# Performance work log

Hardware: AMD Instinct MI355X
Metric: run time of the kernel (lower is better)

The kernel has to match this reference:

```python
import jax, jax.numpy as jnp
import numpy as np

EPS = 1e-7  # K.epsilon()


def setup_inputs() -> dict:
    key = jax.random.key(0)
    k1, k2, k3 = jax.random.split(key, 3)
    B, T, D = 64, 2048, 256
    x = jax.random.normal(k1, (B, T, D), dtype=jnp.float32)
    W = jax.random.normal(k2, (D, D), dtype=jnp.float32) * (1.0 / np.sqrt(D))
    b = jnp.zeros((D,), dtype=jnp.float32)
    uw = jax.random.normal(k3, (D,), dtype=jnp.float32) * (1.0 / np.sqrt(D))
    mask = jnp.ones((B, T), dtype=jnp.int32)
    return {"x": x, "W": W, "b": b, "uw": uw, "mask": mask}


def reference(x, W, b, uw, mask):
    # x: [B, T, D]; W: [D, D]; b, uw: [D]; mask: [B, T]
    eij = jnp.tanh(jnp.einsum('btd,de->bte', x, W) + b)   # [B, T, D]
    eij = jnp.einsum('btd,d->bt', eij, uw)                # [B, T]
    a = jnp.exp(eij) * mask.astype(x.dtype)               # [B, T]
    a = a / (jnp.sum(a, axis=1, keepdims=True) + EPS)     # normalize over time
    return jnp.einsum('btd,bt->bd', x, a)                 # [B, D]
```

## Files before the change

### kernel.cpp

```cpp
#include <hip/hip_runtime.h>
#include <hip/hip_bf16.h>

#define BB 64
#define TT 2048
#define DD 256
#define EPSF 1e-7f
#define ROWS 32
#define XS_STRIDE 264

typedef __attribute__((ext_vector_type(8))) short v8s;
typedef __attribute__((ext_vector_type(4))) float v4f;

__device__ __forceinline__ float bf2f(unsigned short u) {
    union { unsigned int i; float f; } c;
    c.i = ((unsigned int)u) << 16;
    return c.f;
}

__device__ __forceinline__ unsigned int pack2_bf16(float a, float b) {
    union { __hip_bfloat162 h; unsigned int u; } c;
    c.h = __float22bfloat162_rn(make_float2(a, b));
    return c.u;
}

__device__ __forceinline__ float tanh_fast(float x) {
    float e = __expf(2.0f * x);
    return 1.0f - 2.0f / (e + 1.0f);
}

__device__ __forceinline__ unsigned short f2bf_rn(float f) {
    union { __hip_bfloat16 h; unsigned short u; } c;
    c.h = __float2bfloat16(f);
    return c.u;
}

__global__ __launch_bounds__(256) void pack_wt_frag(const float* __restrict__ W,
                                                    unsigned short* __restrict__ Wt) {
    int idx = blockIdx.x * 256 + threadIdx.x;
    int j    = idx & 7;
    int quad = (idx >> 3) & 3;
    int m    = (idx >> 5) & 15;
    int ks   = (idx >> 9) & 7;
    int nt   = idx >> 12;
    int n = nt * 16 + m;
    int k = quad * 8 + ks * 32 + j;
    Wt[idx] = f2bf_rn(W[(size_t)k * DD + n]);
}

__global__ __launch_bounds__(256, 6) void fused_att5(const float* __restrict__ x,
                                                     const unsigned short* __restrict__ Wt,
                                                     const float* __restrict__ bias,
                                                     const float* __restrict__ uw,
                                                     const int* __restrict__ mask,
                                                     float* __restrict__ numpart,
                                                     float* __restrict__ denpart) {
    __shared__ unsigned short xs[ROWS * XS_STRIDE];
    __shared__ float ered[4][ROWS];
    __shared__ float red[4][DD];

    const int tid  = threadIdx.x;
    const int w    = tid >> 6;
    const int lane = tid & 63;
    const int quad = lane >> 4;
    const int m    = lane & 15;
    const long R0  = (long)blockIdx.x * ROWS;
    const long Rw  = R0 + w * 8;

    const size_t blane = (size_t)((m * 4 + quad) * 8);

    float bias_r[4], uw_r[4];
#pragma unroll
    for (int i = 0; i < 4; ++i) {
        int n = (w * 4 + i) * 16 + m;
        bias_r[i] = bias[n];
        uw_r[i]   = uw[n];
    }

    {
        const float* gp = x + Rw * DD + lane * 4;
        unsigned short* sp = xs + (size_t)(w * 8) * XS_STRIDE + lane * 4;
#pragma unroll
        for (int r = 0; r < 8; ++r) {
            float4 v = *(const float4*)(gp + (size_t)r * DD);
            uint2 pp = make_uint2(pack2_bf16(v.x, v.y), pack2_bf16(v.z, v.w));
            *(uint2*)(sp + (size_t)r * XS_STRIDE) = pp;
        }
    }
    __syncthreads();

    float esum[2][4];
#pragma unroll
    for (int mt = 0; mt < 2; ++mt)
#pragma unroll
        for (int r = 0; r < 4; ++r) esum[mt][r] = 0.f;

    v8s a0[8], a1[8];
    {
        const unsigned short* ap0 = xs + (size_t)m * XS_STRIDE + quad * 8;
#pragma unroll
        for (int ks = 0; ks < 8; ++ks) {
            a0[ks] = *(const v8s*)(ap0 + ks * 32);
            a1[ks] = *(const v8s*)(ap0 + 16 * XS_STRIDE + ks * 32);
        }
    }
    v8s bbuf[2][8];
    {
        const unsigned short* bp = Wt + (size_t)(w * 4) * 4096 + blane;
#pragma unroll
        for (int ks = 0; ks < 8; ++ks) bbuf[0][ks] = *(const v8s*)(bp + ks * 512);
    }
#pragma unroll
    for (int i = 0; i < 4; ++i) {
        const int cur = i & 1;
        if (i < 3) {
            const unsigned short* bp = Wt + (size_t)(w * 4 + i + 1) * 4096 + blane;
#pragma unroll
            for (int ks = 0; ks < 8; ++ks) bbuf[cur ^ 1][ks] = *(const v8s*)(bp + ks * 512);
        }
        v4f acc0 = {0.f, 0.f, 0.f, 0.f};
        v4f acc1 = {0.f, 0.f, 0.f, 0.f};
#pragma unroll
        for (int ks = 0; ks < 8; ++ks) {
            acc0 = __builtin_amdgcn_mfma_f32_16x16x32_bf16(a0[ks], bbuf[cur][ks], acc0, 0, 0, 0);
            acc1 = __builtin_amdgcn_mfma_f32_16x16x32_bf16(a1[ks], bbuf[cur][ks], acc1, 0, 0, 0);
        }
#pragma unroll
        for (int r = 0; r < 4; ++r) {
            esum[0][r] += tanh_fast(acc0[r] + bias_r[i]) * uw_r[i];
            esum[1][r] += tanh_fast(acc1[r] + bias_r[i]) * uw_r[i];
        }
    }

#pragma unroll
    for (int o = 1; o < 16; o <<= 1)
#pragma unroll
        for (int mt = 0; mt < 2; ++mt)
#pragma unroll
            for (int r = 0; r < 4; ++r)
                esum[mt][r] += __shfl_xor(esum[mt][r], o, 64);
    if (m == 0) {
#pragma unroll
        for (int mt = 0; mt < 2; ++mt)
#pragma unroll
            for (int r = 0; r < 4; ++r)
                ered[w][mt * 16 + quad * 4 + r] = esum[mt][r];
    }
    __syncthreads();

    const int rl = lane & 31;
    float et = ered[0][rl] + ered[1][rl] + ered[2][rl] + ered[3][rl];
    float p_loc = __expf(et) * (float)mask[R0 + rl];
    float den = p_loc;
#pragma unroll
    for (int o = 1; o < 32; o <<= 1) den += __shfl_xor(den, o, 64);

    float p_all[8];
#pragma unroll
    for (int t = 0; t < 8; ++t) p_all[t] = __shfl(p_loc, w * 8 + t, 64);

    float num[4] = {0.f, 0.f, 0.f, 0.f};
    {
        const unsigned short* xp = xs + (size_t)(w * 8) * XS_STRIDE + lane * 4;
#pragma unroll
        for (int t = 0; t < 8; ++t) {
            uint2 xv = *(const uint2*)(xp + (size_t)t * XS_STRIDE);
            float pt = p_all[t];
            num[0] += pt * bf2f((unsigned short)(xv.x & 0xffffu));
            num[1] += pt * bf2f((unsigned short)(xv.x >> 16));
            num[2] += pt * bf2f((unsigned short)(xv.y & 0xffffu));
            num[3] += pt * bf2f((unsigned short)(xv.y >> 16));
        }
    }

    *(float4*)&red[w][lane * 4] = make_float4(num[0], num[1], num[2], num[3]);
    __syncthreads();
    float s = red[0][tid] + red[1][tid] + red[2][tid] + red[3][tid];
    numpart[(size_t)blockIdx.x * DD + tid] = s;
    if (tid == 0) denpart[blockIdx.x] = den;
}

__global__ __launch_bounds__(256) void finalize(const float* __restrict__ numpart,
                                                const float* __restrict__ denpart,
                                                float* __restrict__ out) {
    __shared__ float4 part[4][64];
    int b = blockIdx.x, t = threadIdx.x;
    int d4 = t & 63;
    int cq = t >> 6;
    float4 s = make_float4(0.f, 0.f, 0.f, 0.f);
    const float* np = numpart + ((size_t)b * 64 + (size_t)cq * 16) * DD + d4 * 4;
#pragma unroll
    for (int c = 0; c < 16; ++c) {
        float4 v = *(const float4*)(np + (size_t)c * DD);
        s.x += v.x; s.y += v.y; s.z += v.z; s.w += v.w;
    }
    part[cq][d4] = s;
    float dp = (t < 64) ? denpart[b * 64 + t] : 0.f;
    __syncthreads();
    if (t < 64) {
#pragma unroll
        for (int o = 1; o < 64; o <<= 1) dp += __shfl_xor(dp, o, 64);
        float4 p0 = part[0][t], p1 = part[1][t], p2 = part[2][t], p3 = part[3][t];
        float inv = 1.0f / (dp + EPSF);
        float4 r;
        r.x = (p0.x + p1.x + p2.x + p3.x) * inv;
        r.y = (p0.y + p1.y + p2.y + p3.y) * inv;
        r.z = (p0.z + p1.z + p2.z + p3.z) * inv;
        r.w = (p0.w + p1.w + p2.w + p3.w) * inv;
        *(float4*)(out + (size_t)b * DD + t * 4) = r;
    }
}

extern "C" void kernel_launch(void* const* d_in, const int* in_sizes, int n_in,
                              void* d_out, int out_size, void* d_ws, size_t ws_size,
                              hipStream_t stream) {
    const float* x    = (const float*)d_in[0];
    const float* W    = (const float*)d_in[1];
    const float* bias = (const float*)d_in[2];
    const float* uw   = (const float*)d_in[3];
    const int*   mask = (const int*)d_in[4];
    float*       out  = (float*)d_out;

    char* ws = (char*)d_ws;
    unsigned short* Wt = (unsigned short*)ws;
    float* numpart     = (float*)(ws + 131072);
    float* denpart     = (float*)(ws + 131072 + 4194304);

    pack_wt_frag<<<dim3(256), dim3(256), 0, stream>>>(W, Wt);
    fused_att5<<<dim3(4096), dim3(256), 0, stream>>>(x, Wt, bias, uw, mask, numpart, denpart);
    finalize<<<dim3(64), dim3(256), 0, stream>>>(numpart, denpart, out);
}
```

Before: 232.2 us.

## Process four row chunks per block with register prefetch and double-buffered LDS

Each block of the fused attention kernel now handles four 32-row chunks instead of one. The next chunk's x rows are prefetched into registers while the current chunk runs its MFMA and softmax-weighted sum, and LDS is double-buffered. Numerator and denominator partials accumulate across chunks, which shrinks the partial buffers and the finalize reduction from 64 to 16 partials per batch. The aim is to hide global load latency and cut partial-write and launch overhead, at the cost of a lower occupancy hint (3 instead of 6), more registers, and a quarter as many blocks.

```diff
diff --git a/kernel.cpp b/kernel.cpp
--- a/kernel.cpp
+++ b/kernel.cpp
@@ -6,6 +6,8 @@
 #define DD 256
 #define EPSF 1e-7f
 #define ROWS 32
+#define CHUNKS 4
+#define BLKROWS (ROWS * CHUNKS)
 #define XS_STRIDE 264
 
 typedef __attribute__((ext_vector_type(8))) short v8s;
@@ -47,14 +49,14 @@
     Wt[idx] = f2bf_rn(W[(size_t)k * DD + n]);
 }
 
-__global__ __launch_bounds__(256, 6) void fused_att5(const float* __restrict__ x,
+__global__ __launch_bounds__(256, 3) void fused_att6(const float* __restrict__ x,
                                                      const unsigned short* __restrict__ Wt,
                                                      const float* __restrict__ bias,
                                                      const float* __restrict__ uw,
                                                      const int* __restrict__ mask,
                                                      float* __restrict__ numpart,
                                                      float* __restrict__ denpart) {
-    __shared__ unsigned short xs[ROWS * XS_STRIDE];
+    __shared__ unsigned short xs[2 * ROWS * XS_STRIDE];
     __shared__ float ered[4][ROWS];
     __shared__ float red[4][DD];
 
@@ -63,8 +65,7 @@
     const int lane = tid & 63;
     const int quad = lane >> 4;
     const int m    = lane & 15;
-    const long R0  = (long)blockIdx.x * ROWS;
-    const long Rw  = R0 + w * 8;
+    const long B0  = (long)blockIdx.x * BLKROWS;
 
     const size_t blane = (size_t)((m * 4 + quad) * 8);
 
@@ -76,32 +77,14 @@
         uw_r[i]   = uw[n];
     }
 
+    float num[4] = {0.f, 0.f, 0.f, 0.f};
+    float denacc = 0.f;
+
+    float4 vreg[8];
     {
-        const float* gp = x + Rw * DD + lane * 4;
-        unsigned short* sp = xs + (size_t)(w * 8) * XS_STRIDE + lane * 4;
-#pragma unroll
-        for (int r = 0; r < 8; ++r) {
-            float4 v = *(const float4*)(gp + (size_t)r * DD);
-            uint2 pp = make_uint2(pack2_bf16(v.x, v.y), pack2_bf16(v.z, v.w));
-            *(uint2*)(sp + (size_t)r * XS_STRIDE) = pp;
-        }
-    }
-    __syncthreads();
-
-    float esum[2][4];
-#pragma unroll
-    for (int mt = 0; mt < 2; ++mt)
-#pragma unroll
-        for (int r = 0; r < 4; ++r) esum[mt][r] = 0.f;
-
-    v8s a0[8], a1[8];
-    {
-        const unsigned short* ap0 = xs + (size_t)m * XS_STRIDE + quad * 8;
-#pragma unroll
-        for (int ks = 0; ks < 8; ++ks) {
-            a0[ks] = *(const v8s*)(ap0 + ks * 32);
-            a1[ks] = *(const v8s*)(ap0 + 16 * XS_STRIDE + ks * 32);
-        }
+        const float* gp = x + (B0 + (size_t)w * 8) * DD + lane * 4;
+#pragma unroll
+        for (int r = 0; r < 8; ++r) vreg[r] = *(const float4*)(gp + (size_t)r * DD);
     }
     v8s bbuf[2][8];
     {
@@ -109,66 +92,104 @@
 #pragma unroll
         for (int ks = 0; ks < 8; ++ks) bbuf[0][ks] = *(const v8s*)(bp + ks * 512);
     }
-#pragma unroll
-    for (int i = 0; i < 4; ++i) {
-        const int cur = i & 1;
-        if (i < 3) {
-            const unsigned short* bp = Wt + (size_t)(w * 4 + i + 1) * 4096 + blane;
-#pragma unroll
-            for (int ks = 0; ks < 8; ++ks) bbuf[cur ^ 1][ks] = *(const v8s*)(bp + ks * 512);
-        }
-        v4f acc0 = {0.f, 0.f, 0.f, 0.f};
-        v4f acc1 = {0.f, 0.f, 0.f, 0.f};
-#pragma unroll
-        for (int ks = 0; ks < 8; ++ks) {
-            acc0 = __builtin_amdgcn_mfma_f32_16x16x32_bf16(a0[ks], bbuf[cur][ks], acc0, 0, 0, 0);
-            acc1 = __builtin_amdgcn_mfma_f32_16x16x32_bf16(a1[ks], bbuf[cur][ks], acc1, 0, 0, 0);
-        }
-#pragma unroll
-        for (int r = 0; r < 4; ++r) {
-            esum[0][r] += tanh_fast(acc0[r] + bias_r[i]) * uw_r[i];
-            esum[1][r] += tanh_fast(acc1[r] + bias_r[i]) * uw_r[i];
-        }
-    }
-
-#pragma unroll
-    for (int o = 1; o < 16; o <<= 1)
+
+    for (int c = 0; c < CHUNKS; ++c) {
+        unsigned short* xb = xs + (size_t)(c & 1) * (ROWS * XS_STRIDE);
+
+        {
+            unsigned short* sp = xb + (size_t)(w * 8) * XS_STRIDE + lane * 4;
+#pragma unroll
+            for (int r = 0; r < 8; ++r) {
+                uint2 pp = make_uint2(pack2_bf16(vreg[r].x, vreg[r].y),
+                                      pack2_bf16(vreg[r].z, vreg[r].w));
+                *(uint2*)(sp + (size_t)r * XS_STRIDE) = pp;
+            }
+        }
+        if (c + 1 < CHUNKS) {
+            const float* gp = x + (B0 + (size_t)(c + 1) * ROWS + (size_t)w * 8) * DD + lane * 4;
+#pragma unroll
+            for (int r = 0; r < 8; ++r) vreg[r] = *(const float4*)(gp + (size_t)r * DD);
+        }
+        __syncthreads();
+
+        v8s a0[8], a1[8];
+        {
+            const unsigned short* ap0 = xb + (size_t)m * XS_STRIDE + quad * 8;
+#pragma unroll
+            for (int ks = 0; ks < 8; ++ks) {
+                a0[ks] = *(const v8s*)(ap0 + ks * 32);
+                a1[ks] = *(const v8s*)(ap0 + 16 * XS_STRIDE + ks * 32);
+            }
+        }
+
+        float esum[2][4];
 #pragma unroll
         for (int mt = 0; mt < 2; ++mt)
 #pragma unroll
-            for (int r = 0; r < 4; ++r)
-                esum[mt][r] += __shfl_xor(esum[mt][r], o, 64);
-    if (m == 0) {
-#pragma unroll
-        for (int mt = 0; mt < 2; ++mt)
-#pragma unroll
-            for (int r = 0; r < 4; ++r)
-                ered[w][mt * 16 + quad * 4 + r] = esum[mt][r];
-    }
-    __syncthreads();
-
-    const int rl = lane & 31;
-    float et = ered[0][rl] + ered[1][rl] + ered[2][rl] + ered[3][rl];
-    float p_loc = __expf(et) * (float)mask[R0 + rl];
-    float den = p_loc;
-#pragma unroll
-    for (int o = 1; o < 32; o <<= 1) den += __shfl_xor(den, o, 64);
-
-    float p_all[8];
-#pragma unroll
-    for (int t = 0; t < 8; ++t) p_all[t] = __shfl(p_loc, w * 8 + t, 64);
-
-    float num[4] = {0.f, 0.f, 0.f, 0.f};
-    {
-        const unsigned short* xp = xs + (size_t)(w * 8) * XS_STRIDE + lane * 4;
-#pragma unroll
-        for (int t = 0; t < 8; ++t) {
-            uint2 xv = *(const uint2*)(xp + (size_t)t * XS_STRIDE);
-            float pt = p_all[t];
-            num[0] += pt * bf2f((unsigned short)(xv.x & 0xffffu));
-            num[1] += pt * bf2f((unsigned short)(xv.x >> 16));
-            num[2] += pt * bf2f((unsigned short)(xv.y & 0xffffu));
-            num[3] += pt * bf2f((unsigned short)(xv.y >> 16));
+            for (int r = 0; r < 4; ++r) esum[mt][r] = 0.f;
+
+#pragma unroll
+        for (int i = 0; i < 4; ++i) {
+            const int cur = i & 1;
+            {
+                const int nxt = (i < 3) ? (w * 4 + i + 1) : (w * 4);
+                const unsigned short* bp = Wt + (size_t)nxt * 4096 + blane;
+#pragma unroll
+                for (int ks = 0; ks < 8; ++ks) bbuf[cur ^ 1][ks] = *(const v8s*)(bp + ks * 512);
+            }
+            v4f acc0 = {0.f, 0.f, 0.f, 0.f};
+            v4f acc1 = {0.f, 0.f, 0.f, 0.f};
+#pragma unroll
+            for (int ks = 0; ks < 8; ++ks) {
+                acc0 = __builtin_amdgcn_mfma_f32_16x16x32_bf16(a0[ks], bbuf[cur][ks], acc0, 0, 0, 0);
+                acc1 = __builtin_amdgcn_mfma_f32_16x16x32_bf16(a1[ks], bbuf[cur][ks], acc1, 0, 0, 0);
+            }
+#pragma unroll
+            for (int r = 0; r < 4; ++r) {
+                esum[0][r] += tanh_fast(acc0[r] + bias_r[i]) * uw_r[i];
+                esum[1][r] += tanh_fast(acc1[r] + bias_r[i]) * uw_r[i];
+            }
+        }
+
+#pragma unroll
+        for (int o = 1; o < 16; o <<= 1)
+#pragma unroll
+            for (int mt = 0; mt < 2; ++mt)
+#pragma unroll
+                for (int r = 0; r < 4; ++r)
+                    esum[mt][r] += __shfl_xor(esum[mt][r], o, 64);
+        if (m == 0) {
+#pragma unroll
+            for (int mt = 0; mt < 2; ++mt)
+#pragma unroll
+                for (int r = 0; r < 4; ++r)
+                    ered[w][mt * 16 + quad * 4 + r] = esum[mt][r];
+        }
+        __syncthreads();
+
+        const int rl = lane & 31;
+        float et = ered[0][rl] + ered[1][rl] + ered[2][rl] + ered[3][rl];
+        float p_loc = __expf(et) * (float)mask[B0 + (size_t)c * ROWS + rl];
+        float den = p_loc;
+#pragma unroll
+        for (int o = 1; o < 32; o <<= 1) den += __shfl_xor(den, o, 64);
+        denacc += den;
+
+        float p_all[8];
+#pragma unroll
+        for (int t = 0; t < 8; ++t) p_all[t] = __shfl(p_loc, w * 8 + t, 64);
+
+        {
+            const unsigned short* xp = xb + (size_t)(w * 8) * XS_STRIDE + lane * 4;
+#pragma unroll
+            for (int t = 0; t < 8; ++t) {
+                uint2 xv = *(const uint2*)(xp + (size_t)t * XS_STRIDE);
+                float pt = p_all[t];
+                num[0] += pt * bf2f((unsigned short)(xv.x & 0xffffu));
+                num[1] += pt * bf2f((unsigned short)(xv.x >> 16));
+                num[2] += pt * bf2f((unsigned short)(xv.y & 0xffffu));
+                num[3] += pt * bf2f((unsigned short)(xv.y >> 16));
+            }
         }
     }
 
@@ -176,7 +197,7 @@
     __syncthreads();
     float s = red[0][tid] + red[1][tid] + red[2][tid] + red[3][tid];
     numpart[(size_t)blockIdx.x * DD + tid] = s;
-    if (tid == 0) denpart[blockIdx.x] = den;
+    if (tid == 0) denpart[blockIdx.x] = denacc;
 }
 
 __global__ __launch_bounds__(256) void finalize(const float* __restrict__ numpart,
@@ -187,18 +208,18 @@
     int d4 = t & 63;
     int cq = t >> 6;
     float4 s = make_float4(0.f, 0.f, 0.f, 0.f);
-    const float* np = numpart + ((size_t)b * 64 + (size_t)cq * 16) * DD + d4 * 4;
-#pragma unroll
-    for (int c = 0; c < 16; ++c) {
+    const float* np = numpart + ((size_t)b * 16 + (size_t)cq * 4) * DD + d4 * 4;
+#pragma unroll
+    for (int c = 0; c < 4; ++c) {
         float4 v = *(const float4*)(np + (size_t)c * DD);
         s.x += v.x; s.y += v.y; s.z += v.z; s.w += v.w;
     }
     part[cq][d4] = s;
-    float dp = (t < 64) ? denpart[b * 64 + t] : 0.f;
+    float dp = denpart[b * 16 + (t & 15)];
     __syncthreads();
     if (t < 64) {
 #pragma unroll
-        for (int o = 1; o < 64; o <<= 1) dp += __shfl_xor(dp, o, 64);
+        for (int o = 1; o < 16; o <<= 1) dp += __shfl_xor(dp, o, 64);
         float4 p0 = part[0][t], p1 = part[1][t], p2 = part[2][t], p3 = part[3][t];
         float inv = 1.0f / (dp + EPSF);
         float4 r;
@@ -223,9 +244,9 @@
     char* ws = (char*)d_ws;
     unsigned short* Wt = (unsigned short*)ws;
     float* numpart     = (float*)(ws + 131072);
-    float* denpart     = (float*)(ws + 131072 + 4194304);
+    float* denpart     = (float*)(ws + 131072 + 1048576);
 
     pack_wt_frag<<<dim3(256), dim3(256), 0, stream>>>(W, Wt);
-    fused_att5<<<dim3(4096), dim3(256), 0, stream>>>(x, Wt, bias, uw, mask, numpart, denpart);
+    fused_att6<<<dim3(1024), dim3(256), 0, stream>>>(x, Wt, bias, uw, mask, numpart, denpart);
     finalize<<<dim3(64), dim3(256), 0, stream>>>(numpart, denpart, out);
 }
```

New measurement: 317.8 us. +36.9%, slower.

## Give each wave its own 16-row tile over all output columns, dropping block syncs

Applied to the files above, without the earlier changes.

Each wavefront now owns 16 rows of x and computes all 256 output columns itself, instead of four waves splitting the columns of a shared 32-row tile. This removes every __syncthreads and the LDS cross-wave reductions. Each wave writes its own numerator and denominator partials, and finalize now reduces 128 partials per batch instead of 64. The cost is that every wave streams the whole packed W (16 column tiles), so W traffic per row doubles. Register pressure also rises, so launch bounds drop to 3 blocks per SIMD, and bias and uw are packed into a float2 table.

```diff
diff --git a/kernel.cpp b/kernel.cpp
--- a/kernel.cpp
+++ b/kernel.cpp
@@ -5,7 +5,7 @@
 #define TT 2048
 #define DD 256
 #define EPSF 1e-7f
-#define ROWS 32
+#define WROWS 16
 #define XS_STRIDE 264
 
 typedef __attribute__((ext_vector_type(8))) short v8s;
@@ -35,7 +35,10 @@
 }
 
 __global__ __launch_bounds__(256) void pack_wt_frag(const float* __restrict__ W,
-                                                    unsigned short* __restrict__ Wt) {
+                                                    const float* __restrict__ bias,
+                                                    const float* __restrict__ uw,
+                                                    unsigned short* __restrict__ Wt,
+                                                    float2* __restrict__ buv) {
     int idx = blockIdx.x * 256 + threadIdx.x;
     int j    = idx & 7;
     int quad = (idx >> 3) & 3;
@@ -45,138 +48,121 @@
     int n = nt * 16 + m;
     int k = quad * 8 + ks * 32 + j;
     Wt[idx] = f2bf_rn(W[(size_t)k * DD + n]);
-}
-
-__global__ __launch_bounds__(256, 6) void fused_att5(const float* __restrict__ x,
+    if (blockIdx.x == 0) buv[threadIdx.x] = make_float2(bias[threadIdx.x], uw[threadIdx.x]);
+}
+
+__global__ __launch_bounds__(256, 3) void fused_att7(const float* __restrict__ x,
                                                      const unsigned short* __restrict__ Wt,
-                                                     const float* __restrict__ bias,
-                                                     const float* __restrict__ uw,
+                                                     const float2* __restrict__ buv,
                                                      const int* __restrict__ mask,
                                                      float* __restrict__ numpart,
                                                      float* __restrict__ denpart) {
-    __shared__ unsigned short xs[ROWS * XS_STRIDE];
-    __shared__ float ered[4][ROWS];
-    __shared__ float red[4][DD];
+    __shared__ unsigned short xs[4 * WROWS * XS_STRIDE];
 
     const int tid  = threadIdx.x;
     const int w    = tid >> 6;
     const int lane = tid & 63;
     const int quad = lane >> 4;
     const int m    = lane & 15;
-    const long R0  = (long)blockIdx.x * ROWS;
-    const long Rw  = R0 + w * 8;
-
-    const size_t blane = (size_t)((m * 4 + quad) * 8);
-
-    float bias_r[4], uw_r[4];
-#pragma unroll
-    for (int i = 0; i < 4; ++i) {
-        int n = (w * 4 + i) * 16 + m;
-        bias_r[i] = bias[n];
-        uw_r[i]   = uw[n];
-    }
-
-    {
-        const float* gp = x + Rw * DD + lane * 4;
-        unsigned short* sp = xs + (size_t)(w * 8) * XS_STRIDE + lane * 4;
-#pragma unroll
-        for (int r = 0; r < 8; ++r) {
-            float4 v = *(const float4*)(gp + (size_t)r * DD);
-            uint2 pp = make_uint2(pack2_bf16(v.x, v.y), pack2_bf16(v.z, v.w));
-            *(uint2*)(sp + (size_t)r * XS_STRIDE) = pp;
-        }
-    }
-    __syncthreads();
-
-    float esum[2][4];
-#pragma unroll
-    for (int mt = 0; mt < 2; ++mt)
-#pragma unroll
-        for (int r = 0; r < 4; ++r) esum[mt][r] = 0.f;
-
-    v8s a0[8], a1[8];
-    {
-        const unsigned short* ap0 = xs + (size_t)m * XS_STRIDE + quad * 8;
-#pragma unroll
-        for (int ks = 0; ks < 8; ++ks) {
-            a0[ks] = *(const v8s*)(ap0 + ks * 32);
-            a1[ks] = *(const v8s*)(ap0 + 16 * XS_STRIDE + ks * 32);
-        }
-    }
+    const int wid  = blockIdx.x * 4 + w;
+    const long Rw0 = (long)wid * WROWS;
+
+    unsigned short* slice = xs + (size_t)(w * WROWS) * XS_STRIDE;
+
+    const unsigned short* wbase = Wt + (size_t)((m * 4 + quad) * 8);
+
     v8s bbuf[2][8];
     {
-        const unsigned short* bp = Wt + (size_t)(w * 4) * 4096 + blane;
-#pragma unroll
-        for (int ks = 0; ks < 8; ++ks) bbuf[0][ks] = *(const v8s*)(bp + ks * 512);
-    }
-#pragma unroll
-    for (int i = 0; i < 4; ++i) {
+        const float* gp = x + Rw0 * DD + lane * 4;
+        unsigned short* sp = slice + lane * 4;
+        float4 vr[8];
+#pragma unroll
+        for (int r = 0; r < 8; ++r) vr[r] = *(const float4*)(gp + (size_t)r * DD);
+#pragma unroll
+        for (int ks = 0; ks < 8; ++ks) bbuf[0][ks] = *(const v8s*)(wbase + ks * 512);
+#pragma unroll
+        for (int r = 0; r < 8; ++r) {
+            uint2 pp = make_uint2(pack2_bf16(vr[r].x, vr[r].y), pack2_bf16(vr[r].z, vr[r].w));
+            *(uint2*)(sp + (size_t)r * XS_STRIDE) = pp;
+        }
+#pragma unroll
+        for (int r = 0; r < 8; ++r) vr[r] = *(const float4*)(gp + (size_t)(8 + r) * DD);
+#pragma unroll
+        for (int r = 0; r < 8; ++r) {
+            uint2 pp = make_uint2(pack2_bf16(vr[r].x, vr[r].y), pack2_bf16(vr[r].z, vr[r].w));
+            *(uint2*)(sp + (size_t)(8 + r) * XS_STRIDE) = pp;
+        }
+    }
+
+    v8s a0[8];
+    {
+        const unsigned short* ap0 = slice + (size_t)m * XS_STRIDE + quad * 8;
+#pragma unroll
+        for (int ks = 0; ks < 8; ++ks) a0[ks] = *(const v8s*)(ap0 + ks * 32);
+    }
+
+    float psum[4] = {0.f, 0.f, 0.f, 0.f};
+#pragma unroll
+    for (int i = 0; i < 16; ++i) {
         const int cur = i & 1;
-        if (i < 3) {
-            const unsigned short* bp = Wt + (size_t)(w * 4 + i + 1) * 4096 + blane;
+        if (i < 15) {
+            const unsigned short* bp = wbase + (size_t)(i + 1) * 4096;
 #pragma unroll
             for (int ks = 0; ks < 8; ++ks) bbuf[cur ^ 1][ks] = *(const v8s*)(bp + ks * 512);
         }
-        v4f acc0 = {0.f, 0.f, 0.f, 0.f};
-        v4f acc1 = {0.f, 0.f, 0.f, 0.f};
-#pragma unroll
-        for (int ks = 0; ks < 8; ++ks) {
-            acc0 = __builtin_amdgcn_mfma_f32_16x16x32_bf16(a0[ks], bbuf[cur][ks], acc0, 0, 0, 0);
-            acc1 = __builtin_amdgcn_mfma_f32_16x16x32_bf16(a1[ks], bbuf[cur][ks], acc1, 0, 0, 0);
-        }
-#pragma unroll
-        for (int r = 0; r < 4; ++r) {
-            esum[0][r] += tanh_fast(acc0[r] + bias_r[i]) * uw_r[i];
-            esum[1][r] += tanh_fast(acc1[r] + bias_r[i]) * uw_r[i];
-        }
+        float2 bu = buv[i * 16 + m];
+        v4f acc = {0.f, 0.f, 0.f, 0.f};
+#pragma unroll
+        for (int ks = 0; ks < 8; ++ks)
+            acc = __builtin_amdgcn_mfma_f32_16x16x32_bf16(a0[ks], bbuf[cur][ks], acc, 0, 0, 0);
+#pragma unroll
+        for (int r = 0; r < 4; ++r)
+            psum[r] += tanh_fast(acc[r] + bu.x) * bu.y;
     }
 
 #pragma unroll
     for (int o = 1; o < 16; o <<= 1)
 #pragma unroll
-        for (int mt = 0; mt < 2; ++mt)
-#pragma unroll
-            for (int r = 0; r < 4; ++r)
-                esum[mt][r] += __shfl_xor(esum[mt][r], o, 64);
-    if (m == 0) {
-#pragma unroll
-        for (int mt = 0; mt < 2; ++mt)
-#pragma unroll
-            for (int r = 0; r < 4; ++r)
-                ered[w][mt * 16 + quad * 4 + r] = esum[mt][r];
-    }
-    __syncthreads();
-
-    const int rl = lane & 31;
-    float et = ered[0][rl] + ered[1][rl] + ered[2][rl] + ered[3][rl];
-    float p_loc = __expf(et) * (float)mask[R0 + rl];
-    float den = p_loc;
-#pragma unroll
-    for (int o = 1; o < 32; o <<= 1) den += __shfl_xor(den, o, 64);
-
-    float p_all[8];
-#pragma unroll
-    for (int t = 0; t < 8; ++t) p_all[t] = __shfl(p_loc, w * 8 + t, 64);
+        for (int r = 0; r < 4; ++r)
+            psum[r] += __shfl_xor(psum[r], o, 64);
+
+    float p_own[4];
+#pragma unroll
+    for (int r = 0; r < 4; ++r)
+        p_own[r] = __expf(psum[r]) * (float)mask[Rw0 + quad * 4 + r];
+    float den = p_own[0] + p_own[1] + p_own[2] + p_own[3];
+    den += __shfl_xor(den, 16, 64);
+    den += __shfl_xor(den, 32, 64);
+
+    float pg[4][4];
+#pragma unroll
+    for (int r = 0; r < 4; ++r) {
+        pg[0][r] = p_own[r];
+        pg[1][r] = __shfl_xor(p_own[r], 16, 64);
+        pg[2][r] = __shfl_xor(p_own[r], 32, 64);
+        pg[3][r] = __shfl_xor(p_own[r], 48, 64);
+    }
 
     float num[4] = {0.f, 0.f, 0.f, 0.f};
     {
-        const unsigned short* xp = xs + (size_t)(w * 8) * XS_STRIDE + lane * 4;
-#pragma unroll
-        for (int t = 0; t < 8; ++t) {
-            uint2 xv = *(const uint2*)(xp + (size_t)t * XS_STRIDE);
-            float pt = p_all[t];
-            num[0] += pt * bf2f((unsigned short)(xv.x & 0xffffu));
-            num[1] += pt * bf2f((unsigned short)(xv.x >> 16));
-            num[2] += pt * bf2f((unsigned short)(xv.y & 0xffffu));
-            num[3] += pt * bf2f((unsigned short)(xv.y >> 16));
-        }
-    }
-
-    *(float4*)&red[w][lane * 4] = make_float4(num[0], num[1], num[2], num[3]);
-    __syncthreads();
-    float s = red[0][tid] + red[1][tid] + red[2][tid] + red[3][tid];
-    numpart[(size_t)blockIdx.x * DD + tid] = s;
-    if (tid == 0) denpart[blockIdx.x] = den;
+        const unsigned short* xp = slice + lane * 4;
+#pragma unroll
+        for (int g = 0; g < 4; ++g) {
+            const int rq = quad ^ g;
+#pragma unroll
+            for (int r = 0; r < 4; ++r) {
+                uint2 xv = *(const uint2*)(xp + (size_t)(rq * 4 + r) * XS_STRIDE);
+                float pt = pg[g][r];
+                num[0] += pt * bf2f((unsigned short)(xv.x & 0xffffu));
+                num[1] += pt * bf2f((unsigned short)(xv.x >> 16));
+                num[2] += pt * bf2f((unsigned short)(xv.y & 0xffffu));
+                num[3] += pt * bf2f((unsigned short)(xv.y >> 16));
+            }
+        }
+    }
+
+    *(float4*)(numpart + (size_t)wid * DD + lane * 4) = make_float4(num[0], num[1], num[2], num[3]);
+    if (lane == 0) denpart[wid] = den;
 }
 
 __global__ __launch_bounds__(256) void finalize(const float* __restrict__ numpart,
@@ -187,16 +173,16 @@
     int d4 = t & 63;
     int cq = t >> 6;
     float4 s = make_float4(0.f, 0.f, 0.f, 0.f);
-    const float* np = numpart + ((size_t)b * 64 + (size_t)cq * 16) * DD + d4 * 4;
-#pragma unroll
-    for (int c = 0; c < 16; ++c) {
+    const float* np = numpart + ((size_t)b * 128 + (size_t)cq * 32) * DD + d4 * 4;
+#pragma unroll
+    for (int c = 0; c < 32; ++c) {
         float4 v = *(const float4*)(np + (size_t)c * DD);
         s.x += v.x; s.y += v.y; s.z += v.z; s.w += v.w;
     }
     part[cq][d4] = s;
-    float dp = (t < 64) ? denpart[b * 64 + t] : 0.f;
     __syncthreads();
     if (t < 64) {
+        float dp = denpart[b * 128 + t] + denpart[b * 128 + 64 + t];
 #pragma unroll
         for (int o = 1; o < 64; o <<= 1) dp += __shfl_xor(dp, o, 64);
         float4 p0 = part[0][t], p1 = part[1][t], p2 = part[2][t], p3 = part[3][t];
@@ -222,10 +208,11 @@
 
     char* ws = (char*)d_ws;
     unsigned short* Wt = (unsigned short*)ws;
-    float* numpart     = (float*)(ws + 131072);
-    float* denpart     = (float*)(ws + 131072 + 4194304);
-
-    pack_wt_frag<<<dim3(256), dim3(256), 0, stream>>>(W, Wt);
-    fused_att5<<<dim3(4096), dim3(256), 0, stream>>>(x, Wt, bias, uw, mask, numpart, denpart);
+    float2* buv        = (float2*)(ws + 131072);
+    float* numpart     = (float*)(ws + 131072 + 2048);
+    float* denpart     = (float*)(ws + 131072 + 2048 + 8388608);
+
+    pack_wt_frag<<<dim3(256), dim3(256), 0, stream>>>(W, bias, uw, Wt, buv);
+    fused_att7<<<dim3(2048), dim3(256), 0, stream>>>(x, Wt, buv, mask, numpart, denpart);
     finalize<<<dim3(64), dim3(256), 0, stream>>>(numpart, denpart, out);
 }
```

Result: slower. 241.1 us (+3.8%).

## Fuse finalize into main kernel via atomics and last-block reduction; streamline tanh

Applied to the files above, without the earlier changes.

Drops the separate finalize kernel and the per-block partial buffers. Each block atomically adds its numerator and denominator into per-batch accumulators, and the last block to finish for a batch, found with a done counter, writes the normalized output. The tanh is rewritten as fma plus exp plus a hardware reciprocal, with 2*bias precomputed in the pack kernel. In exchange it adds a memset launch, float atomic contention (64 blocks per batch on each address), a nondeterministic summation order, and a less precise reciprocal.

```diff
diff --git a/kernel.cpp b/kernel.cpp
--- a/kernel.cpp
+++ b/kernel.cpp
@@ -6,6 +6,7 @@
 #define DD 256
 #define EPSF 1e-7f
 #define ROWS 32
+#define BPB 64
 #define XS_STRIDE 264
 
 typedef __attribute__((ext_vector_type(8))) short v8s;
@@ -23,11 +24,6 @@
     return c.u;
 }
 
-__device__ __forceinline__ float tanh_fast(float x) {
-    float e = __expf(2.0f * x);
-    return 1.0f - 2.0f / (e + 1.0f);
-}
-
 __device__ __forceinline__ unsigned short f2bf_rn(float f) {
     union { __hip_bfloat16 h; unsigned short u; } c;
     c.h = __float2bfloat16(f);
@@ -35,7 +31,10 @@
 }
 
 __global__ __launch_bounds__(256) void pack_wt_frag(const float* __restrict__ W,
-                                                    unsigned short* __restrict__ Wt) {
+                                                    const float* __restrict__ bias,
+                                                    const float* __restrict__ uw,
+                                                    unsigned short* __restrict__ Wt,
+                                                    float2* __restrict__ buv) {
     int idx = blockIdx.x * 256 + threadIdx.x;
     int j    = idx & 7;
     int quad = (idx >> 3) & 3;
@@ -45,18 +44,22 @@
     int n = nt * 16 + m;
     int k = quad * 8 + ks * 32 + j;
     Wt[idx] = f2bf_rn(W[(size_t)k * DD + n]);
-}
-
-__global__ __launch_bounds__(256, 6) void fused_att5(const float* __restrict__ x,
+    if (blockIdx.x == 0)
+        buv[threadIdx.x] = make_float2(2.0f * bias[threadIdx.x], uw[threadIdx.x]);
+}
+
+__global__ __launch_bounds__(256, 6) void fused_att8(const float* __restrict__ x,
                                                      const unsigned short* __restrict__ Wt,
-                                                     const float* __restrict__ bias,
-                                                     const float* __restrict__ uw,
+                                                     const float2* __restrict__ buv,
                                                      const int* __restrict__ mask,
-                                                     float* __restrict__ numpart,
-                                                     float* __restrict__ denpart) {
+                                                     float* __restrict__ numacc,
+                                                     float* __restrict__ denacc,
+                                                     int* __restrict__ done,
+                                                     float* __restrict__ out) {
     __shared__ unsigned short xs[ROWS * XS_STRIDE];
     __shared__ float ered[4][ROWS];
     __shared__ float red[4][DD];
+    __shared__ int lastf;
 
     const int tid  = threadIdx.x;
     const int w    = tid >> 6;
@@ -65,15 +68,16 @@
     const int m    = lane & 15;
     const long R0  = (long)blockIdx.x * ROWS;
     const long Rw  = R0 + w * 8;
+    const int  bb  = blockIdx.x >> 6;
 
     const size_t blane = (size_t)((m * 4 + quad) * 8);
 
-    float bias_r[4], uw_r[4];
+    float bias2_r[4], uw_r[4];
 #pragma unroll
     for (int i = 0; i < 4; ++i) {
-        int n = (w * 4 + i) * 16 + m;
-        bias_r[i] = bias[n];
-        uw_r[i]   = uw[n];
+        float2 bu = buv[(w * 4 + i) * 16 + m];
+        bias2_r[i] = bu.x;
+        uw_r[i]    = bu.y;
     }
 
     {
@@ -126,8 +130,10 @@
         }
 #pragma unroll
         for (int r = 0; r < 4; ++r) {
-            esum[0][r] += tanh_fast(acc0[r] + bias_r[i]) * uw_r[i];
-            esum[1][r] += tanh_fast(acc1[r] + bias_r[i]) * uw_r[i];
+            float r0 = __builtin_amdgcn_rcpf(__expf(__builtin_fmaf(acc0[r], 2.0f, bias2_r[i])) + 1.0f);
+            float r1 = __builtin_amdgcn_rcpf(__expf(__builtin_fmaf(acc1[r], 2.0f, bias2_r[i])) + 1.0f);
+            esum[0][r] = __builtin_fmaf(uw_r[i], __builtin_fmaf(-2.0f, r0, 1.0f), esum[0][r]);
+            esum[1][r] = __builtin_fmaf(uw_r[i], __builtin_fmaf(-2.0f, r1, 1.0f), esum[1][r]);
         }
     }
 
@@ -175,38 +181,20 @@
     *(float4*)&red[w][lane * 4] = make_float4(num[0], num[1], num[2], num[3]);
     __syncthreads();
     float s = red[0][tid] + red[1][tid] + red[2][tid] + red[3][tid];
-    numpart[(size_t)blockIdx.x * DD + tid] = s;
-    if (tid == 0) denpart[blockIdx.x] = den;
-}
-
-__global__ __launch_bounds__(256) void finalize(const float* __restrict__ numpart,
-                                                const float* __restrict__ denpart,
-                                                float* __restrict__ out) {
-    __shared__ float4 part[4][64];
-    int b = blockIdx.x, t = threadIdx.x;
-    int d4 = t & 63;
-    int cq = t >> 6;
-    float4 s = make_float4(0.f, 0.f, 0.f, 0.f);
-    const float* np = numpart + ((size_t)b * 64 + (size_t)cq * 16) * DD + d4 * 4;
-#pragma unroll
-    for (int c = 0; c < 16; ++c) {
-        float4 v = *(const float4*)(np + (size_t)c * DD);
-        s.x += v.x; s.y += v.y; s.z += v.z; s.w += v.w;
-    }
-    part[cq][d4] = s;
-    float dp = (t < 64) ? denpart[b * 64 + t] : 0.f;
-    __syncthreads();
-    if (t < 64) {
-#pragma unroll
-        for (int o = 1; o < 64; o <<= 1) dp += __shfl_xor(dp, o, 64);
-        float4 p0 = part[0][t], p1 = part[1][t], p2 = part[2][t], p3 = part[3][t];
-        float inv = 1.0f / (dp + EPSF);
-        float4 r;
-        r.x = (p0.x + p1.x + p2.x + p3.x) * inv;
-        r.y = (p0.y + p1.y + p2.y + p3.y) * inv;
-        r.z = (p0.z + p1.z + p2.z + p3.z) * inv;
-        r.w = (p0.w + p1.w + p2.w + p3.w) * inv;
-        *(float4*)(out + (size_t)b * DD + t * 4) = r;
+    atomicAdd(&numacc[(size_t)bb * DD + tid], s);
+    if (tid == 0) atomicAdd(&denacc[bb], den);
+    __threadfence();
+    __syncthreads();
+    if (tid == 0) {
+        int old = atomicAdd(&done[bb], 1);
+        lastf = (old == BPB - 1);
+    }
+    __syncthreads();
+    if (lastf) {
+        float dsum = __hip_atomic_load(&denacc[bb], __ATOMIC_RELAXED, __HIP_MEMORY_SCOPE_AGENT);
+        float nsum = __hip_atomic_load(&numacc[(size_t)bb * DD + tid],
+                                       __ATOMIC_RELAXED, __HIP_MEMORY_SCOPE_AGENT);
+        out[(size_t)bb * DD + tid] = nsum / (dsum + EPSF);
     }
 }
 
@@ -222,10 +210,14 @@
 
     char* ws = (char*)d_ws;
     unsigned short* Wt = (unsigned short*)ws;
-    float* numpart     = (float*)(ws + 131072);
-    float* denpart     = (float*)(ws + 131072 + 4194304);
-
-    pack_wt_frag<<<dim3(256), dim3(256), 0, stream>>>(W, Wt);
-    fused_att5<<<dim3(4096), dim3(256), 0, stream>>>(x, Wt, bias, uw, mask, numpart, denpart);
-    finalize<<<dim3(64), dim3(256), 0, stream>>>(numpart, denpart, out);
-}
+    float2* buv        = (float2*)(ws + 131072);
+    float* numacc      = (float*)(ws + 133120);
+    float* denacc      = (float*)(ws + 198656);
+    int*   done        = (int*)(ws + 198912);
+
+    hipMemsetAsync(ws + 133120, 0, 65536 + 256 + 256, stream);
+
+    pack_wt_frag<<<dim3(256), dim3(256), 0, stream>>>(W, bias, uw, Wt, buv);
+    fused_att8<<<dim3(4096), dim3(256), 0, stream>>>(x, Wt, buv, mask,
+                                                     numacc, denacc, done, out);
+}
```

Result: slower. 659.9 us (+184.3%).
